# Kernel optimization log

Hardware: AMD Instinct MI355X
Metric: run time of the kernel (lower is better)

The kernel has to match this reference:

```python
import jax, jax.numpy as jnp
import numpy as np

N_NODES = 100000
N_EDGES = 1000000
D = 128
R = 8


def rgcn_layer(x, src, dst, etype, W, Wroot, b):
    # per-relation transform of all node features: [R, N, D]
    h = jnp.einsum('nd,rde->rne', x, W)
    # gather per-edge messages: [E, D]
    msg = h[etype, src]
    # per-(relation, dst) mean normalization (PyG RGCNConv aggr='mean')
    seg = etype * N_NODES + dst
    deg = jax.ops.segment_sum(jnp.ones((msg.shape[0],), dtype=x.dtype), seg,
                              num_segments=R * N_NODES)
    inv_deg = jnp.where(deg > 0, 1.0 / jnp.maximum(deg, 1.0), 0.0)
    msg = msg * inv_deg[seg][:, None]
    agg = jax.ops.segment_sum(msg, dst, num_segments=N_NODES)
    return agg + x @ Wroot + b


def setup_inputs() -> dict:
    key = jax.random.key(0)
    ks = jax.random.split(key, 10)
    s = 1.0 / np.sqrt(D)
    return {
        'x': jax.random.normal(ks[0], (N_NODES, D), dtype=jnp.float32),
        'edge_index': jax.random.randint(ks[1], (2, N_EDGES), 0, N_NODES, dtype=jnp.int64) if jax.config.jax_enable_x64 else jax.random.randint(ks[1], (2, N_EDGES), 0, N_NODES).astype(jnp.int32),
        'edge_type': jax.random.randint(ks[2], (N_EDGES,), 0, R).astype(jnp.int32),
        'W1': jax.random.uniform(ks[3], (R, D, D), jnp.float32, -s, s),
        'root1': jax.random.uniform(ks[4], (D, D), jnp.float32, -s, s),
        'b1': jnp.zeros((D,), jnp.float32),
        'W2': jax.random.uniform(ks[5], (R, D, D), jnp.float32, -s, s),
        'root2': jax.random.uniform(ks[6], (D, D), jnp.float32, -s, s),
        'b2': jnp.zeros((D,), jnp.float32),
    }


def reference(x, edge_index, edge_type, W1, root1, b1, W2, root2, b2):
    src, dst = edge_index[0], edge_index[1]
    # layer 1: RGCNConv -> ReLU -> Dropout(eval = identity)
    h = jax.nn.relu(rgcn_layer(x, src, dst, edge_type, W1, root1, b1))
    # layer 2 (final): RGCNConv -> ReLU
    h = jax.nn.relu(rgcn_layer(h, src, dst, edge_type, W2, root2, b2))
    return h
```

## Files before the change

kernel.cpp:

```cpp
#include <hip/hip_runtime.h>
#include <hip/hip_bf16.h>

#define NN 100000
#define NE 1000000
#define DD 128
#define RR 8
#define KCAT 1152
#define NBLK 6250

typedef short bf16x8 __attribute__((ext_vector_type(8)));
typedef float f32x4 __attribute__((ext_vector_type(4)));

__device__ __forceinline__ unsigned short f2bf(float f) {
    union { float f; unsigned int u; } c; c.f = f;
    unsigned int u = c.u;
    u += 0x7fffu + ((u >> 16) & 1u);
    return (unsigned short)(u >> 16);
}

__global__ __launch_bounds__(256) void cvt_x_k(const float* __restrict__ in,
                                               unsigned short* __restrict__ out,
                                               int n4) {
    int i = blockIdx.x * 256 + threadIdx.x;
    if (i >= n4) return;
    float4 v = reinterpret_cast<const float4*>(in)[i];
    ushort4 o;
    o.x = f2bf(v.x); o.y = f2bf(v.y); o.z = f2bf(v.z); o.w = f2bf(v.w);
    reinterpret_cast<ushort4*>(out)[i] = o;
}

__global__ __launch_bounds__(256) void cvt_w_k(const float* __restrict__ W1,
                                               const float* __restrict__ r1,
                                               const float* __restrict__ W2,
                                               const float* __restrict__ r2,
                                               unsigned short* __restrict__ wc1,
                                               unsigned short* __restrict__ wc2) {
    int idx = blockIdx.x * 256 + threadIdx.x;
    int l   = idx / (DD * KCAT);
    int rem = idx % (DD * KCAT);
    int e   = rem / KCAT;
    int md  = rem % KCAT;
    int m = md / DD, d = md % DD;
    const float* W = (l == 0) ? W1 : W2;
    const float* rt = (l == 0) ? r1 : r2;
    float v = (m < 8) ? W[(size_t)m * DD * DD + (size_t)d * DD + e]
                      : rt[(size_t)d * DD + e];
    ((l == 0) ? wc1 : wc2)[rem] = f2bf(v);
}

__global__ __launch_bounds__(256) void hist8_k(const int* __restrict__ dst,
                                               const int* __restrict__ et,
                                               unsigned int* __restrict__ deg8) {
    int e = blockIdx.x * 256 + threadIdx.x;
    if (e >= NE) return;
    atomicAdd(&deg8[(size_t)dst[e] * 8 + et[e]], 1u);
}

__global__ __launch_bounds__(256) void offs8_k(const unsigned int* __restrict__ deg8,
                                               unsigned int* __restrict__ counter,
                                               unsigned int* __restrict__ pos8,
                                               unsigned int* __restrict__ segBeg,
                                               unsigned int* __restrict__ segLen,
                                               unsigned int* __restrict__ sorted) {
    int node = blockIdx.x * 256 + threadIdx.x;
    if (node >= NN) return;
    const uint4* dp = reinterpret_cast<const uint4*>(&deg8[(size_t)node * 8]);
    uint4 a = dp[0], b = dp[1];
    unsigned int tot = a.x + a.y + a.z + a.w + b.x + b.y + b.z + b.w;
    unsigned int padTot = (tot + 7u) & ~7u;
    unsigned int base = atomicAdd(counter, padTot);
    unsigned int* pp = &pos8[(size_t)node * 8];
    unsigned int run = base;
    pp[0] = run; run += a.x;  pp[1] = run; run += a.y;
    pp[2] = run; run += a.z;  pp[3] = run; run += a.w;
    pp[4] = run; run += b.x;  pp[5] = run; run += b.y;
    pp[6] = run; run += b.z;  pp[7] = run; run += b.w;
    segBeg[node] = base;
    segLen[node] = padTot;
    for (unsigned int p = base + tot; p < base + padTot; ++p)
        sorted[p] = 0xF00000u;
}

__global__ __launch_bounds__(256) void fill8_k(const int* __restrict__ src,
                                               const int* __restrict__ dst,
                                               const int* __restrict__ et,
                                               const unsigned int* __restrict__ deg8,
                                               unsigned int* __restrict__ pos8,
                                               unsigned int* __restrict__ sorted) {
    int e = blockIdx.x * 256 + threadIdx.x;
    if (e >= NE) return;
    int d = dst[e], r = et[e];
    unsigned int p = atomicAdd(&pos8[(size_t)d * 8 + r], 1u);
    unsigned int dg = deg8[(size_t)d * 8 + r];
    if (dg > 255u) dg = 255u;
    sorted[p] = (unsigned int)src[e] | ((unsigned int)r << 20) | (dg << 24);
}

__global__ __launch_bounds__(256, 4) void fused_k(const unsigned short* __restrict__ xb,
                                                  const unsigned short* __restrict__ wcat,
                                                  const float* __restrict__ bias,
                                                  const unsigned int* __restrict__ sorted,
                                                  const unsigned int* __restrict__ segBeg,
                                                  const unsigned int* __restrict__ segLen,
                                                  unsigned short* __restrict__ obf,
                                                  float* __restrict__ of32,
                                                  int mode) {
    __shared__ unsigned short ldsx[16 * KCAT];
    const int wave = threadIdx.x >> 6;
    const int lane = threadIdx.x & 63;
    const int c16  = lane & 15;
    const int grp  = lane >> 4;
    const int lq   = lane >> 2;
    const int lm   = lane & 3;
    const int blk  = blockIdx.x;
    unsigned int* lds32 = reinterpret_cast<unsigned int*>(ldsx);

    for (int nl = 0; nl < 4; ++nl) {
        const int row  = wave * 4 + nl;
        const int node = blk * 16 + row;
        const int sbase = row * (KCAT / 2);
        const int xorv = row & 7;

#pragma unroll
        for (int r = 0; r < 8; ++r) {
            int slot = (r * 16 + lq) ^ xorv;
            lds32[sbase + slot * 4 + lm] = 0u;
        }
        {
            unsigned int w32 = *reinterpret_cast<const unsigned int*>(
                xb + (size_t)node * DD + lane * 2);
            int slot = (8 * 16 + lq) ^ xorv;
            lds32[sbase + slot * 4 + lm] = w32;
        }

        const unsigned int beg  = segBeg[node];
        const unsigned int lenP = segLen[node];
        const unsigned int* segp = sorted + (unsigned int)__builtin_amdgcn_readfirstlane((int)beg);

        float ax = 0.f, ay = 0.f, scRun = 0.f;
        unsigned int rcur = 15u;

        for (unsigned int j = 0; j < lenP; j += 8) {
            unsigned int pk[8], hv[8];
#pragma unroll
            for (int u = 0; u < 8; ++u) pk[u] = segp[j + u];
#pragma unroll
            for (int u = 0; u < 8; ++u)
                hv[u] = *reinterpret_cast<const unsigned int*>(
                    xb + (size_t)(pk[u] & 0x1FFFFu) * DD + lane * 2);
#pragma unroll
            for (int u = 0; u < 8; ++u) {
                unsigned int r = (pk[u] >> 20) & 0xFu;
                if (r != rcur) {
                    if (rcur < 8u) {
                        unsigned int w32 = ((unsigned int)f2bf(ay * scRun) << 16)
                                         | (unsigned int)f2bf(ax * scRun);
                        int slot = ((int)rcur * 16 + lq) ^ xorv;
                        lds32[sbase + slot * 4 + lm] = w32;
                    }
                    rcur  = r;
                    scRun = __builtin_amdgcn_rcpf((float)(pk[u] >> 24));
                    ax = 0.f; ay = 0.f;
                }
                union { unsigned int u32; float f; } c0, c1;
                c0.u32 = hv[u] << 16;
                c1.u32 = hv[u] & 0xffff0000u;
                ax += c0.f; ay += c1.f;
            }
        }
        if (rcur < 8u) {
            unsigned int w32 = ((unsigned int)f2bf(ay * scRun) << 16)
                             | (unsigned int)f2bf(ax * scRun);
            int slot = ((int)rcur * 16 + lq) ^ xorv;
            lds32[sbase + slot * 4 + lm] = w32;
        }
    }
    __syncthreads();

    const int outb = wave * 32;
    f32x4 acc0 = f32x4{0.f, 0.f, 0.f, 0.f};
    f32x4 acc1 = f32x4{0.f, 0.f, 0.f, 0.f};
    const unsigned short* arow0 = wcat + (size_t)(outb + c16) * KCAT;
    const unsigned short* arow1 = arow0 + 16 * KCAT;
#pragma unroll
    for (int kk = 0; kk < KCAT / 32; ++kk) {
        int slot = (kk * 4 + grp) ^ (c16 & 7);
        bf16x8 b  = *reinterpret_cast<const bf16x8*>(&ldsx[c16 * KCAT + slot * 8]);
        bf16x8 a0 = *reinterpret_cast<const bf16x8*>(arow0 + kk * 32 + grp * 8);
        bf16x8 a1 = *reinterpret_cast<const bf16x8*>(arow1 + kk * 32 + grp * 8);
        acc0 = __builtin_amdgcn_mfma_f32_16x16x32_bf16(a0, b, acc0, 0, 0, 0);
        acc1 = __builtin_amdgcn_mfma_f32_16x16x32_bf16(a1, b, acc1, 0, 0, 0);
    }

    const int node = blk * 16 + c16;
#pragma unroll
    for (int t = 0; t < 2; ++t) {
        const f32x4 acc = t ? acc1 : acc0;
        const int od = outb + t * 16 + grp * 4;
        const float4 bv = *reinterpret_cast<const float4*>(bias + od);
        float o0 = fmaxf(acc[0] + bv.x, 0.f);
        float o1 = fmaxf(acc[1] + bv.y, 0.f);
        float o2 = fmaxf(acc[2] + bv.z, 0.f);
        float o3 = fmaxf(acc[3] + bv.w, 0.f);
        if (mode == 1) {
            union { unsigned short s[4]; uint2 v; } pko;
            pko.s[0] = f2bf(o0); pko.s[1] = f2bf(o1);
            pko.s[2] = f2bf(o2); pko.s[3] = f2bf(o3);
            *reinterpret_cast<uint2*>(obf + (size_t)node * DD + od) = pko.v;
        } else {
            *reinterpret_cast<float4*>(of32 + (size_t)node * DD + od)
                = make_float4(o0, o1, o2, o3);
        }
    }
}

extern "C" void kernel_launch(void* const* d_in, const int* in_sizes, int n_in,
                              void* d_out, int out_size, void* d_ws, size_t ws_size,
                              hipStream_t stream) {
    const float* x  = (const float*)d_in[0];
    const int*   ei = (const int*)d_in[1];
    const int*   et = (const int*)d_in[2];
    const float* W1 = (const float*)d_in[3];
    const float* r1 = (const float*)d_in[4];
    const float* b1 = (const float*)d_in[5];
    const float* W2 = (const float*)d_in[6];
    const float* r2 = (const float*)d_in[7];
    const float* b2 = (const float*)d_in[8];
    float* out = (float*)d_out;

    char* ws = (char*)d_ws;
    unsigned int*   deg8    = (unsigned int*)ws;
    unsigned int*   counter = deg8 + (size_t)NN * 8;
    unsigned int*   pos8    = counter + 64;
    unsigned int*   segBeg  = pos8 + (size_t)NN * 8;
    unsigned int*   segLen  = segBeg + NN;
    unsigned int*   sorted  = segLen + NN;
    unsigned short* wc1     = (unsigned short*)(sorted + NE + 7 * NN);
    unsigned short* wc2     = wc1 + DD * KCAT;
    unsigned short* xbuf    = wc2 + DD * KCAT;
    unsigned short* xbuf2   = xbuf + (size_t)NN * DD;
    size_t need = (size_t)((char*)(xbuf2 + (size_t)NN * DD) - ws);
    if (ws_size < need) return;

    const int* srcv = ei;
    const int* dstv = ei + NE;

    hipMemsetAsync(deg8, 0, ((size_t)NN * 8 + 64) * 4, stream);
    cvt_x_k<<<(NN * DD / 4) / 256, 256, 0, stream>>>(x, xbuf, NN * DD / 4);
    cvt_w_k<<<(2 * DD * KCAT) / 256, 256, 0, stream>>>(W1, r1, W2, r2, wc1, wc2);
    hist8_k<<<(NE + 255) / 256, 256, 0, stream>>>(dstv, et, deg8);
    offs8_k<<<(NN + 255) / 256, 256, 0, stream>>>(deg8, counter, pos8, segBeg, segLen, sorted);
    fill8_k<<<(NE + 255) / 256, 256, 0, stream>>>(srcv, dstv, et, deg8, pos8, sorted);

    fused_k<<<NBLK, 256, 0, stream>>>(xbuf,  wc1, b1, sorted, segBeg, segLen,
                                      xbuf2, (float*)nullptr, 1);
    fused_k<<<NBLK, 256, 0, stream>>>(xbuf2, wc2, b2, sorted, segBeg, segLen,
                                      (unsigned short*)nullptr, out, 2);
}
```

Baseline: 586.4 us.

## Use 8 waves per block, interleave two node gathers per wave with prefetch

The fused gather+MFMA kernel moves from 4 waves to 8 waves per 16-node block. Each wave now aggregates 2 nodes instead of 4, and it interleaves the two nodes' edge streams with a software-pipelined batch prefetch. Edge records are loaded as uint4 vectors. Each wave computes one 16-column MFMA tile instead of two. The aim is more memory-level parallelism and latency hiding in the irregular gather. The cost is a higher register-pressure constraint from launch_bounds(512,8) and weight-row loads spread over more waves.

```diff
diff --git a/kernel.cpp b/kernel.cpp
--- a/kernel.cpp
+++ b/kernel.cpp
@@ -96,7 +96,59 @@
     sorted[p] = (unsigned int)src[e] | ((unsigned int)r << 20) | (dg << 24);
 }
 
-__global__ __launch_bounds__(256, 4) void fused_k(const unsigned short* __restrict__ xb,
+#define LOAD_BATCH(SEGP, J, RA, RB, HV)                                        \
+    do {                                                                       \
+        RA = *reinterpret_cast<const uint4*>((SEGP) + (J));                    \
+        RB = *reinterpret_cast<const uint4*>((SEGP) + (J) + 4);                \
+        HV[0] = *reinterpret_cast<const unsigned int*>(xb + (size_t)(RA.x & 0x1FFFFu) * DD + lane * 2); \
+        HV[1] = *reinterpret_cast<const unsigned int*>(xb + (size_t)(RA.y & 0x1FFFFu) * DD + lane * 2); \
+        HV[2] = *reinterpret_cast<const unsigned int*>(xb + (size_t)(RA.z & 0x1FFFFu) * DD + lane * 2); \
+        HV[3] = *reinterpret_cast<const unsigned int*>(xb + (size_t)(RA.w & 0x1FFFFu) * DD + lane * 2); \
+        HV[4] = *reinterpret_cast<const unsigned int*>(xb + (size_t)(RB.x & 0x1FFFFu) * DD + lane * 2); \
+        HV[5] = *reinterpret_cast<const unsigned int*>(xb + (size_t)(RB.y & 0x1FFFFu) * DD + lane * 2); \
+        HV[6] = *reinterpret_cast<const unsigned int*>(xb + (size_t)(RB.z & 0x1FFFFu) * DD + lane * 2); \
+        HV[7] = *reinterpret_cast<const unsigned int*>(xb + (size_t)(RB.w & 0x1FFFFu) * DD + lane * 2); \
+    } while (0)
+
+#define PROC_ONE(PKV, HVV, AX, AY, RC, SC, SB, XV)                             \
+    do {                                                                       \
+        unsigned int r_ = ((PKV) >> 20) & 0xFu;                                \
+        if (r_ != (RC)) {                                                      \
+            if ((RC) < 8u) {                                                   \
+                unsigned int w_ = ((unsigned int)f2bf((AY) * (SC)) << 16)      \
+                                | (unsigned int)f2bf((AX) * (SC));             \
+                lds32[(SB) + ((((int)(RC) * 16 + lq) ^ (XV)) << 2) + lm] = w_; \
+            }                                                                  \
+            RC = r_; SC = __builtin_amdgcn_rcpf((float)((PKV) >> 24));         \
+            AX = 0.f; AY = 0.f;                                                \
+        }                                                                      \
+        union { unsigned int u; float f; } lo_, hi_;                           \
+        lo_.u = (HVV) << 16; hi_.u = (HVV) & 0xffff0000u;                      \
+        AX += lo_.f; AY += hi_.f;                                              \
+    } while (0)
+
+#define PROC_BATCH(RA, RB, HV, AX, AY, RC, SC, SB, XV)                         \
+    do {                                                                       \
+        PROC_ONE(RA.x, HV[0], AX, AY, RC, SC, SB, XV);                         \
+        PROC_ONE(RA.y, HV[1], AX, AY, RC, SC, SB, XV);                         \
+        PROC_ONE(RA.z, HV[2], AX, AY, RC, SC, SB, XV);                         \
+        PROC_ONE(RA.w, HV[3], AX, AY, RC, SC, SB, XV);                         \
+        PROC_ONE(RB.x, HV[4], AX, AY, RC, SC, SB, XV);                         \
+        PROC_ONE(RB.y, HV[5], AX, AY, RC, SC, SB, XV);                         \
+        PROC_ONE(RB.z, HV[6], AX, AY, RC, SC, SB, XV);                         \
+        PROC_ONE(RB.w, HV[7], AX, AY, RC, SC, SB, XV);                         \
+    } while (0)
+
+#define FLUSH_RUN(AX, AY, RC, SC, SB, XV)                                      \
+    do {                                                                       \
+        if ((RC) < 8u) {                                                       \
+            unsigned int w_ = ((unsigned int)f2bf((AY) * (SC)) << 16)          \
+                            | (unsigned int)f2bf((AX) * (SC));                 \
+            lds32[(SB) + ((((int)(RC) * 16 + lq) ^ (XV)) << 2) + lm] = w_;     \
+        }                                                                      \
+    } while (0)
+
+__global__ __launch_bounds__(512, 8) void fused_k(const unsigned short* __restrict__ xb,
                                                   const unsigned short* __restrict__ wcat,
                                                   const float* __restrict__ bias,
                                                   const unsigned int* __restrict__ sorted,
@@ -115,102 +167,80 @@
     const int blk  = blockIdx.x;
     unsigned int* lds32 = reinterpret_cast<unsigned int*>(ldsx);
 
-    for (int nl = 0; nl < 4; ++nl) {
-        const int row  = wave * 4 + nl;
-        const int node = blk * 16 + row;
-        const int sbase = row * (KCAT / 2);
-        const int xorv = row & 7;
+    const int row0 = wave * 2, row1 = wave * 2 + 1;
+    const int node0 = blk * 16 + row0, node1 = blk * 16 + row1;
+    const int sb0 = row0 * (KCAT / 2), sb1 = row1 * (KCAT / 2);
+    const int xv0 = row0 & 7, xv1 = row1 & 7;
 
 #pragma unroll
-        for (int r = 0; r < 8; ++r) {
-            int slot = (r * 16 + lq) ^ xorv;
-            lds32[sbase + slot * 4 + lm] = 0u;
+    for (int r = 0; r < 8; ++r) {
+        lds32[sb0 + (((r * 16 + lq) ^ xv0) << 2) + lm] = 0u;
+        lds32[sb1 + (((r * 16 + lq) ^ xv1) << 2) + lm] = 0u;
+    }
+    lds32[sb0 + (((128 + lq) ^ xv0) << 2) + lm] =
+        *reinterpret_cast<const unsigned int*>(xb + (size_t)node0 * DD + lane * 2);
+    lds32[sb1 + (((128 + lq) ^ xv1) << 2) + lm] =
+        *reinterpret_cast<const unsigned int*>(xb + (size_t)node1 * DD + lane * 2);
+
+    const unsigned int* segp0 = sorted +
+        (unsigned int)__builtin_amdgcn_readfirstlane((int)segBeg[node0]);
+    const unsigned int* segp1 = sorted +
+        (unsigned int)__builtin_amdgcn_readfirstlane((int)segBeg[node1]);
+    const unsigned int len0 =
+        (unsigned int)__builtin_amdgcn_readfirstlane((int)segLen[node0]);
+    const unsigned int len1 =
+        (unsigned int)__builtin_amdgcn_readfirstlane((int)segLen[node1]);
+
+    unsigned int j0 = 0, j1 = 0;
+    float ax0 = 0.f, ay0 = 0.f, ax1 = 0.f, ay1 = 0.f, sc0 = 0.f, sc1 = 0.f;
+    unsigned int rc0 = 15u, rc1 = 15u;
+    uint4 ra0, rb0, ra1, rb1;
+    unsigned int hv0[8], hv1[8];
+
+    bool v0 = (j0 < len0), v1 = (j1 < len1);
+    if (v0) LOAD_BATCH(segp0, j0, ra0, rb0, hv0);
+    if (v1) LOAD_BATCH(segp1, j1, ra1, rb1, hv1);
+    while (v0 || v1) {
+        if (v0) {
+            PROC_BATCH(ra0, rb0, hv0, ax0, ay0, rc0, sc0, sb0, xv0);
+            j0 += 8; v0 = (j0 < len0);
+            if (v0) LOAD_BATCH(segp0, j0, ra0, rb0, hv0);
         }
-        {
-            unsigned int w32 = *reinterpret_cast<const unsigned int*>(
-                xb + (size_t)node * DD + lane * 2);
-            int slot = (8 * 16 + lq) ^ xorv;
-            lds32[sbase + slot * 4 + lm] = w32;
+        if (v1) {
+            PROC_BATCH(ra1, rb1, hv1, ax1, ay1, rc1, sc1, sb1, xv1);
+            j1 += 8; v1 = (j1 < len1);
+            if (v1) LOAD_BATCH(segp1, j1, ra1, rb1, hv1);
         }
-
-        const unsigned int beg  = segBeg[node];
-        const unsigned int lenP = segLen[node];
-        const unsigned int* segp = sorted + (unsigned int)__builtin_amdgcn_readfirstlane((int)beg);
-
-        float ax = 0.f, ay = 0.f, scRun = 0.f;
-        unsigned int rcur = 15u;
-
-        for (unsigned int j = 0; j < lenP; j += 8) {
-            unsigned int pk[8], hv[8];
-#pragma unroll
-            for (int u = 0; u < 8; ++u) pk[u] = segp[j + u];
-#pragma unroll
-            for (int u = 0; u < 8; ++u)
-                hv[u] = *reinterpret_cast<const unsigned int*>(
-                    xb + (size_t)(pk[u] & 0x1FFFFu) * DD + lane * 2);
-#pragma unroll
-            for (int u = 0; u < 8; ++u) {
-                unsigned int r = (pk[u] >> 20) & 0xFu;
-                if (r != rcur) {
-                    if (rcur < 8u) {
-                        unsigned int w32 = ((unsigned int)f2bf(ay * scRun) << 16)
-                                         | (unsigned int)f2bf(ax * scRun);
-                        int slot = ((int)rcur * 16 + lq) ^ xorv;
-                        lds32[sbase + slot * 4 + lm] = w32;
-                    }
-                    rcur  = r;
-                    scRun = __builtin_amdgcn_rcpf((float)(pk[u] >> 24));
-                    ax = 0.f; ay = 0.f;
-                }
-                union { unsigned int u32; float f; } c0, c1;
-                c0.u32 = hv[u] << 16;
-                c1.u32 = hv[u] & 0xffff0000u;
-                ax += c0.f; ay += c1.f;
-            }
-        }
-        if (rcur < 8u) {
-            unsigned int w32 = ((unsigned int)f2bf(ay * scRun) << 16)
-                             | (unsigned int)f2bf(ax * scRun);
-            int slot = ((int)rcur * 16 + lq) ^ xorv;
-            lds32[sbase + slot * 4 + lm] = w32;
-        }
-    }
+    }
+    FLUSH_RUN(ax0, ay0, rc0, sc0, sb0, xv0);
+    FLUSH_RUN(ax1, ay1, rc1, sc1, sb1, xv1);
     __syncthreads();
 
-    const int outb = wave * 32;
-    f32x4 acc0 = f32x4{0.f, 0.f, 0.f, 0.f};
-    f32x4 acc1 = f32x4{0.f, 0.f, 0.f, 0.f};
-    const unsigned short* arow0 = wcat + (size_t)(outb + c16) * KCAT;
-    const unsigned short* arow1 = arow0 + 16 * KCAT;
+    f32x4 acc = f32x4{0.f, 0.f, 0.f, 0.f};
+    const unsigned short* arow = wcat + (size_t)(wave * 16 + c16) * KCAT;
 #pragma unroll
     for (int kk = 0; kk < KCAT / 32; ++kk) {
         int slot = (kk * 4 + grp) ^ (c16 & 7);
-        bf16x8 b  = *reinterpret_cast<const bf16x8*>(&ldsx[c16 * KCAT + slot * 8]);
-        bf16x8 a0 = *reinterpret_cast<const bf16x8*>(arow0 + kk * 32 + grp * 8);
-        bf16x8 a1 = *reinterpret_cast<const bf16x8*>(arow1 + kk * 32 + grp * 8);
-        acc0 = __builtin_amdgcn_mfma_f32_16x16x32_bf16(a0, b, acc0, 0, 0, 0);
-        acc1 = __builtin_amdgcn_mfma_f32_16x16x32_bf16(a1, b, acc1, 0, 0, 0);
+        bf16x8 b = *reinterpret_cast<const bf16x8*>(&ldsx[c16 * KCAT + slot * 8]);
+        bf16x8 a = *reinterpret_cast<const bf16x8*>(arow + kk * 32 + grp * 8);
+        acc = __builtin_amdgcn_mfma_f32_16x16x32_bf16(a, b, acc, 0, 0, 0);
     }
 
     const int node = blk * 16 + c16;
-#pragma unroll
-    for (int t = 0; t < 2; ++t) {
-        const f32x4 acc = t ? acc1 : acc0;
-        const int od = outb + t * 16 + grp * 4;
-        const float4 bv = *reinterpret_cast<const float4*>(bias + od);
-        float o0 = fmaxf(acc[0] + bv.x, 0.f);
-        float o1 = fmaxf(acc[1] + bv.y, 0.f);
-        float o2 = fmaxf(acc[2] + bv.z, 0.f);
-        float o3 = fmaxf(acc[3] + bv.w, 0.f);
-        if (mode == 1) {
-            union { unsigned short s[4]; uint2 v; } pko;
-            pko.s[0] = f2bf(o0); pko.s[1] = f2bf(o1);
-            pko.s[2] = f2bf(o2); pko.s[3] = f2bf(o3);
-            *reinterpret_cast<uint2*>(obf + (size_t)node * DD + od) = pko.v;
-        } else {
-            *reinterpret_cast<float4*>(of32 + (size_t)node * DD + od)
-                = make_float4(o0, o1, o2, o3);
-        }
+    const int od = wave * 16 + grp * 4;
+    const float4 bv = *reinterpret_cast<const float4*>(bias + od);
+    float o0 = fmaxf(acc[0] + bv.x, 0.f);
+    float o1 = fmaxf(acc[1] + bv.y, 0.f);
+    float o2 = fmaxf(acc[2] + bv.z, 0.f);
+    float o3 = fmaxf(acc[3] + bv.w, 0.f);
+    if (mode == 1) {
+        union { unsigned short s[4]; uint2 v; } pko;
+        pko.s[0] = f2bf(o0); pko.s[1] = f2bf(o1);
+        pko.s[2] = f2bf(o2); pko.s[3] = f2bf(o3);
+        *reinterpret_cast<uint2*>(obf + (size_t)node * DD + od) = pko.v;
+    } else {
+        *reinterpret_cast<float4*>(of32 + (size_t)node * DD + od)
+            = make_float4(o0, o1, o2, o3);
     }
 }
 
@@ -252,8 +282,8 @@
     offs8_k<<<(NN + 255) / 256, 256, 0, stream>>>(deg8, counter, pos8, segBeg, segLen, sorted);
     fill8_k<<<(NE + 255) / 256, 256, 0, stream>>>(srcv, dstv, et, deg8, pos8, sorted);
 
-    fused_k<<<NBLK, 256, 0, stream>>>(xbuf,  wc1, b1, sorted, segBeg, segLen,
+    fused_k<<<NBLK, 512, 0, stream>>>(xbuf,  wc1, b1, sorted, segBeg, segLen,
                                       xbuf2, (float*)nullptr, 1);
-    fused_k<<<NBLK, 256, 0, stream>>>(xbuf2, wc2, b2, sorted, segBeg, segLen,
+    fused_k<<<NBLK, 512, 0, stream>>>(xbuf2, wc2, b2, sorted, segBeg, segLen,
                                       (unsigned short*)nullptr, out, 2);
 }
```

Result: no change. 587.0 us (+0.1%).

## Aggregate edge messages with LDS float atomics in a per-node bucket layout

Applied to the files above, without the earlier changes.

Edges are now bucketed per destination node only, not per (node, relation). The fused kernel processes four edges at a time per wave, with each 16-lane group gathering a 16-byte chunk and scaling it. Results are accumulated into fp32 LDS slots with atomicAdd, then converted to bf16 when the MFMA operands are built. Blocks go to 512 threads with one 16-column MFMA tile per wave, and padded records point at a zero row. This drops the per-relation sorted order and the run-tracking logic, and gives wider gathers per lane. In exchange it pays for LDS atomic contention, a larger LDS footprint (about 110KB) that limits occupancy, and a full LDS zeroing pass.

```diff
diff --git a/kernel.cpp b/kernel.cpp
--- a/kernel.cpp
+++ b/kernel.cpp
@@ -7,6 +7,10 @@
 #define RR 8
 #define KCAT 1152
 #define NBLK 6250
+#define ZROW NN
+#define CH_STRIDE 12
+#define SL_STRIDE 192
+#define ROW_STRIDE 1732
 
 typedef short bf16x8 __attribute__((ext_vector_type(8)));
 typedef float f32x4 __attribute__((ext_vector_type(4)));
@@ -56,161 +60,140 @@
     atomicAdd(&deg8[(size_t)dst[e] * 8 + et[e]], 1u);
 }
 
-__global__ __launch_bounds__(256) void offs8_k(const unsigned int* __restrict__ deg8,
-                                               unsigned int* __restrict__ counter,
-                                               unsigned int* __restrict__ pos8,
-                                               unsigned int* __restrict__ segBeg,
-                                               unsigned int* __restrict__ segLen,
-                                               unsigned int* __restrict__ sorted) {
+__global__ __launch_bounds__(256) void offs_k(const unsigned int* __restrict__ deg8,
+                                              unsigned int* __restrict__ counter,
+                                              unsigned int* __restrict__ posN,
+                                              unsigned int* __restrict__ segBeg,
+                                              unsigned int* __restrict__ segLen,
+                                              unsigned int* __restrict__ sorted) {
     int node = blockIdx.x * 256 + threadIdx.x;
     if (node >= NN) return;
     const uint4* dp = reinterpret_cast<const uint4*>(&deg8[(size_t)node * 8]);
     uint4 a = dp[0], b = dp[1];
     unsigned int tot = a.x + a.y + a.z + a.w + b.x + b.y + b.z + b.w;
-    unsigned int padTot = (tot + 7u) & ~7u;
+    unsigned int padTot = (tot + 3u) & ~3u;
     unsigned int base = atomicAdd(counter, padTot);
-    unsigned int* pp = &pos8[(size_t)node * 8];
-    unsigned int run = base;
-    pp[0] = run; run += a.x;  pp[1] = run; run += a.y;
-    pp[2] = run; run += a.z;  pp[3] = run; run += a.w;
-    pp[4] = run; run += b.x;  pp[5] = run; run += b.y;
-    pp[6] = run; run += b.z;  pp[7] = run; run += b.w;
+    posN[node]   = base;
     segBeg[node] = base;
     segLen[node] = padTot;
+    const unsigned int dummy = (unsigned int)ZROW | (0u << 17) | (1u << 20);
     for (unsigned int p = base + tot; p < base + padTot; ++p)
-        sorted[p] = 0xF00000u;
-}
-
-__global__ __launch_bounds__(256) void fill8_k(const int* __restrict__ src,
-                                               const int* __restrict__ dst,
-                                               const int* __restrict__ et,
-                                               const unsigned int* __restrict__ deg8,
-                                               unsigned int* __restrict__ pos8,
-                                               unsigned int* __restrict__ sorted) {
+        sorted[p] = dummy;
+}
+
+__global__ __launch_bounds__(256) void fill_k(const int* __restrict__ src,
+                                              const int* __restrict__ dst,
+                                              const int* __restrict__ et,
+                                              const unsigned int* __restrict__ deg8,
+                                              unsigned int* __restrict__ posN,
+                                              unsigned int* __restrict__ sorted) {
     int e = blockIdx.x * 256 + threadIdx.x;
     if (e >= NE) return;
     int d = dst[e], r = et[e];
-    unsigned int p = atomicAdd(&pos8[(size_t)d * 8 + r], 1u);
+    unsigned int p = atomicAdd(&posN[d], 1u);
     unsigned int dg = deg8[(size_t)d * 8 + r];
-    if (dg > 255u) dg = 255u;
-    sorted[p] = (unsigned int)src[e] | ((unsigned int)r << 20) | (dg << 24);
-}
-
-__global__ __launch_bounds__(256, 4) void fused_k(const unsigned short* __restrict__ xb,
-                                                  const unsigned short* __restrict__ wcat,
-                                                  const float* __restrict__ bias,
-                                                  const unsigned int* __restrict__ sorted,
-                                                  const unsigned int* __restrict__ segBeg,
-                                                  const unsigned int* __restrict__ segLen,
-                                                  unsigned short* __restrict__ obf,
-                                                  float* __restrict__ of32,
-                                                  int mode) {
-    __shared__ unsigned short ldsx[16 * KCAT];
+    if (dg > 2047u) dg = 2047u;
+    sorted[p] = (unsigned int)src[e] | ((unsigned int)r << 17) | (dg << 20);
+}
+
+__global__ __launch_bounds__(512) void fused_k(const unsigned short* __restrict__ xb,
+                                               const unsigned short* __restrict__ wcat,
+                                               const float* __restrict__ bias,
+                                               const unsigned int* __restrict__ sorted,
+                                               const unsigned int* __restrict__ segBeg,
+                                               const unsigned int* __restrict__ segLen,
+                                               unsigned short* __restrict__ obf,
+                                               float* __restrict__ of32,
+                                               int mode) {
+    __shared__ float ldsf[16 * ROW_STRIDE];
     const int wave = threadIdx.x >> 6;
     const int lane = threadIdx.x & 63;
     const int c16  = lane & 15;
     const int grp  = lane >> 4;
-    const int lq   = lane >> 2;
-    const int lm   = lane & 3;
     const int blk  = blockIdx.x;
-    unsigned int* lds32 = reinterpret_cast<unsigned int*>(ldsx);
-
-    for (int nl = 0; nl < 4; ++nl) {
-        const int row  = wave * 4 + nl;
+
+    for (int i = threadIdx.x; i < 16 * ROW_STRIDE; i += 512)
+        ldsf[i] = 0.f;
+    __syncthreads();
+
+    for (int nl = 0; nl < 2; ++nl) {
+        const int row  = wave * 2 + nl;
         const int node = blk * 16 + row;
-        const int sbase = row * (KCAT / 2);
-        const int xorv = row & 7;
-
-#pragma unroll
-        for (int r = 0; r < 8; ++r) {
-            int slot = (r * 16 + lq) ^ xorv;
-            lds32[sbase + slot * 4 + lm] = 0u;
-        }
+        const float* ldsrow = ldsf + row * ROW_STRIDE;
+
         {
             unsigned int w32 = *reinterpret_cast<const unsigned int*>(
                 xb + (size_t)node * DD + lane * 2);
-            int slot = (8 * 16 + lq) ^ xorv;
-            lds32[sbase + slot * 4 + lm] = w32;
+            union { unsigned int u; float f; } lo, hi;
+            lo.u = w32 << 16; hi.u = w32 & 0xffff0000u;
+            int e = lane * 2;
+            float* p = const_cast<float*>(ldsrow) + 8 * SL_STRIDE
+                     + (e >> 3) * CH_STRIDE + (e & 7);
+            p[0] = lo.f; p[1] = hi.f;
         }
 
-        const unsigned int beg  = segBeg[node];
-        const unsigned int lenP = segLen[node];
-        const unsigned int* segp = sorted + (unsigned int)__builtin_amdgcn_readfirstlane((int)beg);
-
-        float ax = 0.f, ay = 0.f, scRun = 0.f;
-        unsigned int rcur = 15u;
-
-        for (unsigned int j = 0; j < lenP; j += 8) {
-            unsigned int pk[8], hv[8];
+        const unsigned int beg =
+            (unsigned int)__builtin_amdgcn_readfirstlane((int)segBeg[node]);
+        const unsigned int lenP =
+            (unsigned int)__builtin_amdgcn_readfirstlane((int)segLen[node]);
+        const unsigned int* segp = sorted + beg;
+
+        for (unsigned int j = 0; j < lenP; j += 4) {
+            unsigned int rec = segp[j + grp];
+            unsigned int srcN = rec & 0x1FFFFu;
+            unsigned int r    = (rec >> 17) & 7u;
+            float sc = __builtin_amdgcn_rcpf((float)(rec >> 20));
+            uint4 q = *reinterpret_cast<const uint4*>(
+                xb + (size_t)srcN * DD + c16 * 8);
+            float* basep = const_cast<float*>(ldsrow) + r * SL_STRIDE
+                         + c16 * CH_STRIDE;
+            union { unsigned int u; float f; } lo, hi;
 #pragma unroll
-            for (int u = 0; u < 8; ++u) pk[u] = segp[j + u];
-#pragma unroll
-            for (int u = 0; u < 8; ++u)
-                hv[u] = *reinterpret_cast<const unsigned int*>(
-                    xb + (size_t)(pk[u] & 0x1FFFFu) * DD + lane * 2);
-#pragma unroll
-            for (int u = 0; u < 8; ++u) {
-                unsigned int r = (pk[u] >> 20) & 0xFu;
-                if (r != rcur) {
-                    if (rcur < 8u) {
-                        unsigned int w32 = ((unsigned int)f2bf(ay * scRun) << 16)
-                                         | (unsigned int)f2bf(ax * scRun);
-                        int slot = ((int)rcur * 16 + lq) ^ xorv;
-                        lds32[sbase + slot * 4 + lm] = w32;
-                    }
-                    rcur  = r;
-                    scRun = __builtin_amdgcn_rcpf((float)(pk[u] >> 24));
-                    ax = 0.f; ay = 0.f;
-                }
-                union { unsigned int u32; float f; } c0, c1;
-                c0.u32 = hv[u] << 16;
-                c1.u32 = hv[u] & 0xffff0000u;
-                ax += c0.f; ay += c1.f;
+            for (int k = 0; k < 4; ++k) {
+                unsigned int w32 = (&q.x)[k];
+                lo.u = w32 << 16; hi.u = w32 & 0xffff0000u;
+                atomicAdd(basep + 2 * k,     lo.f * sc);
+                atomicAdd(basep + 2 * k + 1, hi.f * sc);
             }
-        }
-        if (rcur < 8u) {
-            unsigned int w32 = ((unsigned int)f2bf(ay * scRun) << 16)
-                             | (unsigned int)f2bf(ax * scRun);
-            int slot = ((int)rcur * 16 + lq) ^ xorv;
-            lds32[sbase + slot * 4 + lm] = w32;
         }
     }
     __syncthreads();
 
-    const int outb = wave * 32;
-    f32x4 acc0 = f32x4{0.f, 0.f, 0.f, 0.f};
-    f32x4 acc1 = f32x4{0.f, 0.f, 0.f, 0.f};
-    const unsigned short* arow0 = wcat + (size_t)(outb + c16) * KCAT;
-    const unsigned short* arow1 = arow0 + 16 * KCAT;
+    f32x4 acc = f32x4{0.f, 0.f, 0.f, 0.f};
+    const unsigned short* arow = wcat + (size_t)(wave * 16 + c16) * KCAT;
+    const float* brow = ldsf + c16 * ROW_STRIDE;
 #pragma unroll
     for (int kk = 0; kk < KCAT / 32; ++kk) {
-        int slot = (kk * 4 + grp) ^ (c16 & 7);
-        bf16x8 b  = *reinterpret_cast<const bf16x8*>(&ldsx[c16 * KCAT + slot * 8]);
-        bf16x8 a0 = *reinterpret_cast<const bf16x8*>(arow0 + kk * 32 + grp * 8);
-        bf16x8 a1 = *reinterpret_cast<const bf16x8*>(arow1 + kk * 32 + grp * 8);
-        acc0 = __builtin_amdgcn_mfma_f32_16x16x32_bf16(a0, b, acc0, 0, 0, 0);
-        acc1 = __builtin_amdgcn_mfma_f32_16x16x32_bf16(a1, b, acc1, 0, 0, 0);
+        int g8 = kk * 4 + grp;
+        const float* cp = brow + (g8 >> 4) * SL_STRIDE + (g8 & 15) * CH_STRIDE;
+        f32x4 f0 = *reinterpret_cast<const f32x4*>(cp);
+        f32x4 f1 = *reinterpret_cast<const f32x4*>(cp + 4);
+        unsigned int p0, p1, p2, p3;
+        asm volatile("v_cvt_pk_bf16_f32 %0, %1, %2" : "=v"(p0) : "v"(f0[0]), "v"(f0[1]));
+        asm volatile("v_cvt_pk_bf16_f32 %0, %1, %2" : "=v"(p1) : "v"(f0[2]), "v"(f0[3]));
+        asm volatile("v_cvt_pk_bf16_f32 %0, %1, %2" : "=v"(p2) : "v"(f1[0]), "v"(f1[1]));
+        asm volatile("v_cvt_pk_bf16_f32 %0, %1, %2" : "=v"(p3) : "v"(f1[2]), "v"(f1[3]));
+        union { unsigned int u[4]; bf16x8 v; } bfr;
+        bfr.u[0] = p0; bfr.u[1] = p1; bfr.u[2] = p2; bfr.u[3] = p3;
+        bf16x8 a = *reinterpret_cast<const bf16x8*>(arow + kk * 32 + grp * 8);
+        acc = __builtin_amdgcn_mfma_f32_16x16x32_bf16(a, bfr.v, acc, 0, 0, 0);
     }
 
     const int node = blk * 16 + c16;
-#pragma unroll
-    for (int t = 0; t < 2; ++t) {
-        const f32x4 acc = t ? acc1 : acc0;
-        const int od = outb + t * 16 + grp * 4;
-        const float4 bv = *reinterpret_cast<const float4*>(bias + od);
-        float o0 = fmaxf(acc[0] + bv.x, 0.f);
-        float o1 = fmaxf(acc[1] + bv.y, 0.f);
-        float o2 = fmaxf(acc[2] + bv.z, 0.f);
-        float o3 = fmaxf(acc[3] + bv.w, 0.f);
-        if (mode == 1) {
-            union { unsigned short s[4]; uint2 v; } pko;
-            pko.s[0] = f2bf(o0); pko.s[1] = f2bf(o1);
-            pko.s[2] = f2bf(o2); pko.s[3] = f2bf(o3);
-            *reinterpret_cast<uint2*>(obf + (size_t)node * DD + od) = pko.v;
-        } else {
-            *reinterpret_cast<float4*>(of32 + (size_t)node * DD + od)
-                = make_float4(o0, o1, o2, o3);
-        }
+    const int od = wave * 16 + grp * 4;
+    const float4 bv = *reinterpret_cast<const float4*>(bias + od);
+    float o0 = fmaxf(acc[0] + bv.x, 0.f);
+    float o1 = fmaxf(acc[1] + bv.y, 0.f);
+    float o2 = fmaxf(acc[2] + bv.z, 0.f);
+    float o3 = fmaxf(acc[3] + bv.w, 0.f);
+    if (mode == 1) {
+        union { unsigned short s[4]; uint2 v; } pko;
+        pko.s[0] = f2bf(o0); pko.s[1] = f2bf(o1);
+        pko.s[2] = f2bf(o2); pko.s[3] = f2bf(o3);
+        *reinterpret_cast<uint2*>(obf + (size_t)node * DD + od) = pko.v;
+    } else {
+        *reinterpret_cast<float4*>(of32 + (size_t)node * DD + od)
+            = make_float4(o0, o1, o2, o3);
     }
 }
 
@@ -231,29 +214,31 @@
     char* ws = (char*)d_ws;
     unsigned int*   deg8    = (unsigned int*)ws;
     unsigned int*   counter = deg8 + (size_t)NN * 8;
-    unsigned int*   pos8    = counter + 64;
-    unsigned int*   segBeg  = pos8 + (size_t)NN * 8;
+    unsigned int*   posN    = counter + 64;
+    unsigned int*   segBeg  = posN + NN;
     unsigned int*   segLen  = segBeg + NN;
     unsigned int*   sorted  = segLen + NN;
-    unsigned short* wc1     = (unsigned short*)(sorted + NE + 7 * NN);
+    unsigned short* wc1     = (unsigned short*)(sorted + NE + 3 * NN);
     unsigned short* wc2     = wc1 + DD * KCAT;
     unsigned short* xbuf    = wc2 + DD * KCAT;
-    unsigned short* xbuf2   = xbuf + (size_t)NN * DD;
-    size_t need = (size_t)((char*)(xbuf2 + (size_t)NN * DD) - ws);
+    unsigned short* xbuf2   = xbuf + (size_t)(NN + 1) * DD;
+    size_t need = (size_t)((char*)(xbuf2 + (size_t)(NN + 1) * DD) - ws);
     if (ws_size < need) return;
 
     const int* srcv = ei;
     const int* dstv = ei + NE;
 
     hipMemsetAsync(deg8, 0, ((size_t)NN * 8 + 64) * 4, stream);
+    hipMemsetAsync(xbuf  + (size_t)NN * DD, 0, DD * 2, stream);
+    hipMemsetAsync(xbuf2 + (size_t)NN * DD, 0, DD * 2, stream);
     cvt_x_k<<<(NN * DD / 4) / 256, 256, 0, stream>>>(x, xbuf, NN * DD / 4);
     cvt_w_k<<<(2 * DD * KCAT) / 256, 256, 0, stream>>>(W1, r1, W2, r2, wc1, wc2);
     hist8_k<<<(NE + 255) / 256, 256, 0, stream>>>(dstv, et, deg8);
-    offs8_k<<<(NN + 255) / 256, 256, 0, stream>>>(deg8, counter, pos8, segBeg, segLen, sorted);
-    fill8_k<<<(NE + 255) / 256, 256, 0, stream>>>(srcv, dstv, et, deg8, pos8, sorted);
-
-    fused_k<<<NBLK, 256, 0, stream>>>(xbuf,  wc1, b1, sorted, segBeg, segLen,
+    offs_k<<<(NN + 255) / 256, 256, 0, stream>>>(deg8, counter, posN, segBeg, segLen, sorted);
+    fill_k<<<(NE + 255) / 256, 256, 0, stream>>>(srcv, dstv, et, deg8, posN, sorted);
+
+    fused_k<<<NBLK, 512, 0, stream>>>(xbuf,  wc1, b1, sorted, segBeg, segLen,
                                       xbuf2, (float*)nullptr, 1);
-    fused_k<<<NBLK, 256, 0, stream>>>(xbuf2, wc2, b2, sorted, segBeg, segLen,
+    fused_k<<<NBLK, 512, 0, stream>>>(xbuf2, wc2, b2, sorted, segBeg, segLen,
                                       (unsigned short*)nullptr, out, 2);
 }
```

After: 2.201 ms. 275% more time.

## Split message passing into source-ordered scatter pass plus contiguous dst-sorted aggregation

Applied to the files above, without the earlier changes.

Replaces the random per-edge gather in the fused aggregation kernel with a two-phase scheme. A spread kernel walks edges grouped by source, reads each source row once in roughly sequential order, scales it by the inverse relation degree and writes the bf16 message into a dst-sorted edge buffer. The aggregation kernel then streams those messages contiguously. This targets gather locality but adds a full E×D bf16 write and read per layer, which can be chunked when workspace is short. The aggregation block grows to 512 threads with one 16-column MFMA tile per wave.

```diff
diff --git a/kernel.cpp b/kernel.cpp
--- a/kernel.cpp
+++ b/kernel.cpp
@@ -4,9 +4,7 @@
 #define NN 100000
 #define NE 1000000
 #define DD 128
-#define RR 8
 #define KCAT 1152
-#define NBLK 6250
 
 typedef short bf16x8 __attribute__((ext_vector_type(8)));
 typedef float f32x4 __attribute__((ext_vector_type(4)));
@@ -48,27 +46,31 @@
     ((l == 0) ? wc1 : wc2)[rem] = f2bf(v);
 }
 
-__global__ __launch_bounds__(256) void hist8_k(const int* __restrict__ dst,
-                                               const int* __restrict__ et,
-                                               unsigned int* __restrict__ deg8) {
+__global__ __launch_bounds__(256) void hist_k(const int* __restrict__ src,
+                                              const int* __restrict__ dst,
+                                              const int* __restrict__ et,
+                                              unsigned int* __restrict__ deg8,
+                                              unsigned int* __restrict__ posS) {
     int e = blockIdx.x * 256 + threadIdx.x;
     if (e >= NE) return;
     atomicAdd(&deg8[(size_t)dst[e] * 8 + et[e]], 1u);
-}
-
-__global__ __launch_bounds__(256) void offs8_k(const unsigned int* __restrict__ deg8,
-                                               unsigned int* __restrict__ counter,
-                                               unsigned int* __restrict__ pos8,
-                                               unsigned int* __restrict__ segBeg,
-                                               unsigned int* __restrict__ segLen,
-                                               unsigned int* __restrict__ sorted) {
+    atomicAdd(&posS[src[e]], 1u);
+}
+
+__global__ __launch_bounds__(256) void offs_k(const unsigned int* __restrict__ deg8,
+                                              unsigned int* __restrict__ cnts,
+                                              unsigned int* __restrict__ pos8,
+                                              unsigned int* __restrict__ posS,
+                                              unsigned int* __restrict__ segBeg,
+                                              unsigned int* __restrict__ segLen,
+                                              unsigned int CAP, int nch) {
     int node = blockIdx.x * 256 + threadIdx.x;
     if (node >= NN) return;
     const uint4* dp = reinterpret_cast<const uint4*>(&deg8[(size_t)node * 8]);
     uint4 a = dp[0], b = dp[1];
     unsigned int tot = a.x + a.y + a.z + a.w + b.x + b.y + b.z + b.w;
-    unsigned int padTot = (tot + 7u) & ~7u;
-    unsigned int base = atomicAdd(counter, padTot);
+    int c = (nch == 2 && node >= NN / 2) ? 1 : 0;
+    unsigned int base = atomicAdd(&cnts[c], tot) + (unsigned int)c * CAP;
     unsigned int* pp = &pos8[(size_t)node * 8];
     unsigned int run = base;
     pp[0] = run; run += a.x;  pp[1] = run; run += a.y;
@@ -76,35 +78,86 @@
     pp[4] = run; run += b.x;  pp[5] = run; run += b.y;
     pp[6] = run; run += b.z;  pp[7] = run; run += b.w;
     segBeg[node] = base;
-    segLen[node] = padTot;
-    for (unsigned int p = base + tot; p < base + padTot; ++p)
-        sorted[p] = 0xF00000u;
-}
-
-__global__ __launch_bounds__(256) void fill8_k(const int* __restrict__ src,
-                                               const int* __restrict__ dst,
-                                               const int* __restrict__ et,
-                                               const unsigned int* __restrict__ deg8,
-                                               unsigned int* __restrict__ pos8,
-                                               unsigned int* __restrict__ sorted) {
+    segLen[node] = tot;
+    unsigned int q0 = atomicAdd(&cnts[2], posS[node]);
+    posS[node] = q0;
+}
+
+__global__ __launch_bounds__(256) void fill_k(const int* __restrict__ src,
+                                              const int* __restrict__ dst,
+                                              const int* __restrict__ et,
+                                              const unsigned int* __restrict__ deg8,
+                                              unsigned int* __restrict__ pos8,
+                                              unsigned int* __restrict__ posS,
+                                              unsigned int* __restrict__ recA,
+                                              unsigned int* __restrict__ recB,
+                                              unsigned char* __restrict__ recD) {
     int e = blockIdx.x * 256 + threadIdx.x;
     if (e >= NE) return;
-    int d = dst[e], r = et[e];
+    int s = src[e], d = dst[e], r = et[e];
     unsigned int p = atomicAdd(&pos8[(size_t)d * 8 + r], 1u);
+    recD[p] = (unsigned char)r;
+    unsigned int q = atomicAdd(&posS[s], 1u);
     unsigned int dg = deg8[(size_t)d * 8 + r];
-    if (dg > 255u) dg = 255u;
-    sorted[p] = (unsigned int)src[e] | ((unsigned int)r << 20) | (dg << 24);
-}
-
-__global__ __launch_bounds__(256, 4) void fused_k(const unsigned short* __restrict__ xb,
-                                                  const unsigned short* __restrict__ wcat,
-                                                  const float* __restrict__ bias,
-                                                  const unsigned int* __restrict__ sorted,
-                                                  const unsigned int* __restrict__ segBeg,
-                                                  const unsigned int* __restrict__ segLen,
-                                                  unsigned short* __restrict__ obf,
-                                                  float* __restrict__ of32,
-                                                  int mode) {
+    if (dg > 2047u) dg = 2047u;
+    recA[q] = (unsigned int)s | (dg << 17);
+    recB[q] = p;
+}
+
+__global__ __launch_bounds__(512) void spread_k(const unsigned short* __restrict__ xb,
+                                                const unsigned int* __restrict__ recA,
+                                                const unsigned int* __restrict__ recB,
+                                                unsigned short* __restrict__ y,
+                                                unsigned int chunkOff, unsigned int CAP) {
+    const int gw   = blockIdx.x * 8 + (threadIdx.x >> 6);
+    const int lane = threadIdx.x & 63;
+    const int b0   = gw * 200;
+
+    for (int b = 0; b < 200; b += 8) {
+        int j = b0 + b;
+        uint4 a0 = *reinterpret_cast<const uint4*>(recA + j);
+        uint4 a1 = *reinterpret_cast<const uint4*>(recA + j + 4);
+        uint4 s0 = *reinterpret_cast<const uint4*>(recB + j);
+        uint4 s1 = *reinterpret_cast<const uint4*>(recB + j + 4);
+        unsigned int pk[8] = {a0.x, a0.y, a0.z, a0.w, a1.x, a1.y, a1.z, a1.w};
+        unsigned int sl[8] = {s0.x, s0.y, s0.z, s0.w, s1.x, s1.y, s1.z, s1.w};
+        unsigned int hv[8];
+#pragma unroll
+        for (int u = 0; u < 8; ++u) {
+            unsigned int rel = sl[u] - chunkOff;
+            if (rel < CAP)
+                hv[u] = *reinterpret_cast<const unsigned int*>(
+                    xb + (size_t)(pk[u] & 0x1FFFFu) * DD + lane * 2);
+        }
+#pragma unroll
+        for (int u = 0; u < 8; ++u) {
+            unsigned int rel = sl[u] - chunkOff;
+            if (rel < CAP) {
+                float sc = __builtin_amdgcn_rcpf((float)(pk[u] >> 17));
+                union { unsigned int u32; float f; } lo, hi;
+                lo.u32 = hv[u] << 16; hi.u32 = hv[u] & 0xffff0000u;
+                float flo = lo.f * sc, fhi = hi.f * sc;
+                unsigned int w32;
+                asm volatile("v_cvt_pk_bf16_f32 %0, %1, %2"
+                             : "=v"(w32) : "v"(flo), "v"(fhi));
+                __builtin_nontemporal_store(w32,
+                    reinterpret_cast<unsigned int*>(y + (size_t)rel * DD + lane * 2));
+            }
+        }
+    }
+}
+
+__global__ __launch_bounds__(512) void agg_k(const unsigned short* __restrict__ xb,
+                                             const unsigned short* __restrict__ wcat,
+                                             const float* __restrict__ bias,
+                                             const unsigned char* __restrict__ recD,
+                                             const unsigned int* __restrict__ segBeg,
+                                             const unsigned int* __restrict__ segLen,
+                                             const unsigned short* __restrict__ y,
+                                             unsigned int chunkOff, int nodeLo,
+                                             unsigned short* __restrict__ obf,
+                                             float* __restrict__ of32,
+                                             int mode) {
     __shared__ unsigned short ldsx[16 * KCAT];
     const int wave = threadIdx.x >> 6;
     const int lane = threadIdx.x & 63;
@@ -115,102 +168,85 @@
     const int blk  = blockIdx.x;
     unsigned int* lds32 = reinterpret_cast<unsigned int*>(ldsx);
 
-    for (int nl = 0; nl < 4; ++nl) {
-        const int row  = wave * 4 + nl;
-        const int node = blk * 16 + row;
+    for (int nl = 0; nl < 2; ++nl) {
+        const int row  = wave * 2 + nl;
+        const int node = nodeLo + blk * 16 + row;
         const int sbase = row * (KCAT / 2);
         const int xorv = row & 7;
 
 #pragma unroll
-        for (int r = 0; r < 8; ++r) {
-            int slot = (r * 16 + lq) ^ xorv;
-            lds32[sbase + slot * 4 + lm] = 0u;
-        }
-        {
-            unsigned int w32 = *reinterpret_cast<const unsigned int*>(
-                xb + (size_t)node * DD + lane * 2);
-            int slot = (8 * 16 + lq) ^ xorv;
-            lds32[sbase + slot * 4 + lm] = w32;
-        }
-
-        const unsigned int beg  = segBeg[node];
-        const unsigned int lenP = segLen[node];
-        const unsigned int* segp = sorted + (unsigned int)__builtin_amdgcn_readfirstlane((int)beg);
-
-        float ax = 0.f, ay = 0.f, scRun = 0.f;
-        unsigned int rcur = 15u;
-
-        for (unsigned int j = 0; j < lenP; j += 8) {
-            unsigned int pk[8], hv[8];
-#pragma unroll
-            for (int u = 0; u < 8; ++u) pk[u] = segp[j + u];
+        for (int r = 0; r < 8; ++r)
+            lds32[sbase + (((r * 16 + lq) ^ xorv) << 2) + lm] = 0u;
+        lds32[sbase + (((128 + lq) ^ xorv) << 2) + lm] =
+            *reinterpret_cast<const unsigned int*>(xb + (size_t)node * DD + lane * 2);
+
+        const unsigned int beg = segBeg[node];
+        const unsigned int len = segLen[node];
+        const unsigned char* rp = recD + beg;
+        const unsigned short* yb = y + (size_t)(beg - chunkOff) * DD;
+
+        float ax = 0.f, ay = 0.f;
+        unsigned int rc = 15u;
+        for (unsigned int j = 0; j < len; j += 8) {
+            int n = (int)(len - j); if (n > 8) n = 8;
+            unsigned int hv[8]; unsigned char rr[8];
 #pragma unroll
             for (int u = 0; u < 8; ++u)
-                hv[u] = *reinterpret_cast<const unsigned int*>(
-                    xb + (size_t)(pk[u] & 0x1FFFFu) * DD + lane * 2);
-#pragma unroll
-            for (int u = 0; u < 8; ++u) {
-                unsigned int r = (pk[u] >> 20) & 0xFu;
-                if (r != rcur) {
-                    if (rcur < 8u) {
-                        unsigned int w32 = ((unsigned int)f2bf(ay * scRun) << 16)
-                                         | (unsigned int)f2bf(ax * scRun);
-                        int slot = ((int)rcur * 16 + lq) ^ xorv;
-                        lds32[sbase + slot * 4 + lm] = w32;
+                if (u < n) {
+                    rr[u] = rp[j + u];
+                    hv[u] = *reinterpret_cast<const unsigned int*>(
+                        yb + (size_t)(j + u) * DD + lane * 2);
+                }
+#pragma unroll
+            for (int u = 0; u < 8; ++u)
+                if (u < n) {
+                    unsigned int r = rr[u];
+                    if (r != rc) {
+                        if (rc < 8u) {
+                            unsigned int w32 = ((unsigned int)f2bf(ay) << 16)
+                                             | (unsigned int)f2bf(ax);
+                            lds32[sbase + ((((int)rc * 16 + lq) ^ xorv) << 2) + lm] = w32;
+                        }
+                        rc = r; ax = 0.f; ay = 0.f;
                     }
-                    rcur  = r;
-                    scRun = __builtin_amdgcn_rcpf((float)(pk[u] >> 24));
-                    ax = 0.f; ay = 0.f;
+                    union { unsigned int u32; float f; } lo, hi;
+                    lo.u32 = hv[u] << 16; hi.u32 = hv[u] & 0xffff0000u;
+                    ax += lo.f; ay += hi.f;
                 }
-                union { unsigned int u32; float f; } c0, c1;
-                c0.u32 = hv[u] << 16;
-                c1.u32 = hv[u] & 0xffff0000u;
-                ax += c0.f; ay += c1.f;
-            }
-        }
-        if (rcur < 8u) {
-            unsigned int w32 = ((unsigned int)f2bf(ay * scRun) << 16)
-                             | (unsigned int)f2bf(ax * scRun);
-            int slot = ((int)rcur * 16 + lq) ^ xorv;
-            lds32[sbase + slot * 4 + lm] = w32;
+        }
+        if (rc < 8u) {
+            unsigned int w32 = ((unsigned int)f2bf(ay) << 16)
+                             | (unsigned int)f2bf(ax);
+            lds32[sbase + ((((int)rc * 16 + lq) ^ xorv) << 2) + lm] = w32;
         }
     }
     __syncthreads();
 
-    const int outb = wave * 32;
-    f32x4 acc0 = f32x4{0.f, 0.f, 0.f, 0.f};
-    f32x4 acc1 = f32x4{0.f, 0.f, 0.f, 0.f};
-    const unsigned short* arow0 = wcat + (size_t)(outb + c16) * KCAT;
-    const unsigned short* arow1 = arow0 + 16 * KCAT;
+    f32x4 acc = f32x4{0.f, 0.f, 0.f, 0.f};
+    const unsigned short* arow = wcat + (size_t)(wave * 16 + c16) * KCAT;
 #pragma unroll
     for (int kk = 0; kk < KCAT / 32; ++kk) {
         int slot = (kk * 4 + grp) ^ (c16 & 7);
-        bf16x8 b  = *reinterpret_cast<const bf16x8*>(&ldsx[c16 * KCAT + slot * 8]);
-        bf16x8 a0 = *reinterpret_cast<const bf16x8*>(arow0 + kk * 32 + grp * 8);
-        bf16x8 a1 = *reinterpret_cast<const bf16x8*>(arow1 + kk * 32 + grp * 8);
-        acc0 = __builtin_amdgcn_mfma_f32_16x16x32_bf16(a0, b, acc0, 0, 0, 0);
-        acc1 = __builtin_amdgcn_mfma_f32_16x16x32_bf16(a1, b, acc1, 0, 0, 0);
-    }
-
-    const int node = blk * 16 + c16;
-#pragma unroll
-    for (int t = 0; t < 2; ++t) {
-        const f32x4 acc = t ? acc1 : acc0;
-        const int od = outb + t * 16 + grp * 4;
-        const float4 bv = *reinterpret_cast<const float4*>(bias + od);
-        float o0 = fmaxf(acc[0] + bv.x, 0.f);
-        float o1 = fmaxf(acc[1] + bv.y, 0.f);
-        float o2 = fmaxf(acc[2] + bv.z, 0.f);
-        float o3 = fmaxf(acc[3] + bv.w, 0.f);
-        if (mode == 1) {
-            union { unsigned short s[4]; uint2 v; } pko;
-            pko.s[0] = f2bf(o0); pko.s[1] = f2bf(o1);
-            pko.s[2] = f2bf(o2); pko.s[3] = f2bf(o3);
-            *reinterpret_cast<uint2*>(obf + (size_t)node * DD + od) = pko.v;
-        } else {
-            *reinterpret_cast<float4*>(of32 + (size_t)node * DD + od)
-                = make_float4(o0, o1, o2, o3);
-        }
+        bf16x8 b = *reinterpret_cast<const bf16x8*>(&ldsx[c16 * KCAT + slot * 8]);
+        bf16x8 a = *reinterpret_cast<const bf16x8*>(arow + kk * 32 + grp * 8);
+        acc = __builtin_amdgcn_mfma_f32_16x16x32_bf16(a, b, acc, 0, 0, 0);
+    }
+
+    const int node = nodeLo + blk * 16 + c16;
+    const int od = wave * 16 + grp * 4;
+    const float4 bv = *reinterpret_cast<const float4*>(bias + od);
+    float o0 = fmaxf(acc[0] + bv.x, 0.f);
+    float o1 = fmaxf(acc[1] + bv.y, 0.f);
+    float o2 = fmaxf(acc[2] + bv.z, 0.f);
+    float o3 = fmaxf(acc[3] + bv.w, 0.f);
+    if (mode == 1) {
+        union { unsigned short s[4]; uint2 v; } pko;
+        pko.s[0] = f2bf(o0); pko.s[1] = f2bf(o1);
+        pko.s[2] = f2bf(o2); pko.s[3] = f2bf(o3);
+        *reinterpret_cast<uint2*>(obf + (size_t)node * DD + od) = pko.v;
+    } else {
+        *reinterpret_cast<float4*>(of32 + (size_t)node * DD + od)
+            = make_float4(o0, o1, o2, o3);
     }
 }
 
@@ -229,31 +265,61 @@
     float* out = (float*)d_out;
 
     char* ws = (char*)d_ws;
-    unsigned int*   deg8    = (unsigned int*)ws;
-    unsigned int*   counter = deg8 + (size_t)NN * 8;
-    unsigned int*   pos8    = counter + 64;
-    unsigned int*   segBeg  = pos8 + (size_t)NN * 8;
-    unsigned int*   segLen  = segBeg + NN;
-    unsigned int*   sorted  = segLen + NN;
-    unsigned short* wc1     = (unsigned short*)(sorted + NE + 7 * NN);
-    unsigned short* wc2     = wc1 + DD * KCAT;
-    unsigned short* xbuf    = wc2 + DD * KCAT;
-    unsigned short* xbuf2   = xbuf + (size_t)NN * DD;
-    size_t need = (size_t)((char*)(xbuf2 + (size_t)NN * DD) - ws);
-    if (ws_size < need) return;
+    unsigned int*   deg8   = (unsigned int*)ws;
+    unsigned int*   cnts   = deg8 + (size_t)NN * 8;
+    unsigned int*   posS   = cnts + 64;
+    unsigned int*   pos8   = posS + NN;
+    unsigned int*   segBeg = pos8 + (size_t)NN * 8;
+    unsigned int*   segLen = segBeg + NN;
+    unsigned int*   recA   = segLen + NN;
+    unsigned int*   recB   = recA + NE;
+    unsigned short* wc1    = (unsigned short*)(recB + NE);
+    unsigned short* wc2    = wc1 + DD * KCAT;
+    unsigned short* xbuf   = wc2 + DD * KCAT;
+    unsigned short* xbuf2  = xbuf + (size_t)NN * DD;
+    size_t fixedEnd = (size_t)((char*)(xbuf2 + (size_t)NN * DD) - ws);
+    fixedEnd = (fixedEnd + 255) & ~(size_t)255;
+
+    if (ws_size < fixedEnd + 1024) return;
+    size_t avail = ws_size - fixedEnd - 512;
+    int nch; unsigned int CAP;
+    if (avail >= (size_t)NE * 257) { nch = 1; CAP = NE; }
+    else {
+        nch = 2;
+        CAP = (unsigned int)(avail / 258);
+        if (CAP < 530000u) return;
+        if (CAP > NE) CAP = NE;
+    }
+    unsigned char* recD = (unsigned char*)(ws + fixedEnd);
+    size_t yOff = (fixedEnd + (size_t)nch * CAP + 255) & ~(size_t)255;
+    unsigned short* y = (unsigned short*)(ws + yOff);
 
     const int* srcv = ei;
     const int* dstv = ei + NE;
 
-    hipMemsetAsync(deg8, 0, ((size_t)NN * 8 + 64) * 4, stream);
+    hipMemsetAsync(deg8, 0, (size_t)NN * 8 * 4 + 256 + (size_t)NN * 4, stream);
     cvt_x_k<<<(NN * DD / 4) / 256, 256, 0, stream>>>(x, xbuf, NN * DD / 4);
     cvt_w_k<<<(2 * DD * KCAT) / 256, 256, 0, stream>>>(W1, r1, W2, r2, wc1, wc2);
-    hist8_k<<<(NE + 255) / 256, 256, 0, stream>>>(dstv, et, deg8);
-    offs8_k<<<(NN + 255) / 256, 256, 0, stream>>>(deg8, counter, pos8, segBeg, segLen, sorted);
-    fill8_k<<<(NE + 255) / 256, 256, 0, stream>>>(srcv, dstv, et, deg8, pos8, sorted);
-
-    fused_k<<<NBLK, 256, 0, stream>>>(xbuf,  wc1, b1, sorted, segBeg, segLen,
-                                      xbuf2, (float*)nullptr, 1);
-    fused_k<<<NBLK, 256, 0, stream>>>(xbuf2, wc2, b2, sorted, segBeg, segLen,
-                                      (unsigned short*)nullptr, out, 2);
-}
+    hist_k<<<(NE + 255) / 256, 256, 0, stream>>>(srcv, dstv, et, deg8, posS);
+    offs_k<<<(NN + 255) / 256, 256, 0, stream>>>(deg8, cnts, pos8, posS,
+                                                 segBeg, segLen, CAP, nch);
+    fill_k<<<(NE + 255) / 256, 256, 0, stream>>>(srcv, dstv, et, deg8, pos8, posS,
+                                                 recA, recB, recD);
+
+    const int nodesPer = NN / nch;
+    const int aggBlocks = nodesPer / 16;
+    for (int layer = 0; layer < 2; ++layer) {
+        const unsigned short* in = layer ? xbuf2 : xbuf;
+        const unsigned short* wc = layer ? wc2 : wc1;
+        const float* bb = layer ? b2 : b1;
+        for (int c = 0; c < nch; ++c) {
+            unsigned int chunkOff = (unsigned int)c * CAP;
+            spread_k<<<625, 512, 0, stream>>>(in, recA, recB, y, chunkOff, CAP);
+            agg_k<<<aggBlocks, 512, 0, stream>>>(in, wc, bb, recD, segBeg, segLen,
+                                                 y, chunkOff, c * nodesPer,
+                                                 layer ? (unsigned short*)nullptr : xbuf2,
+                                                 layer ? out : (float*)nullptr,
+                                                 layer ? 2 : 1);
+        }
+    }
+}
```

Result: slower. 2.141 ms (median of 4 runs) (+265.1%).
